# Kernel tuning notes

Hardware: AMD Instinct MI355X
Metric: run time of the kernel (lower is better)

Reference implementation:

```python
import jax, jax.numpy as jnp
import numpy as np
from jax import lax

B, V, C, H, W = 2, 8, 64, 128, 128
A = 256
C3 = 3 * C + 2  # 194 input channels for refine/confidence branches
CO = 3 * C      # 192 output channels of branch_refine
GROUPS = 8      # _group_count(192, 8) == 8
HID = max(4, CO // 4)  # 48 hidden channels in ChannelGate2d


def _conv3(x, w, b):
    y = lax.conv_general_dilated(x, w, (1, 1), 'SAME',
                                 dimension_numbers=('NCHW', 'OIHW', 'NCHW'))
    return y + b[None, :, None, None]


def _group_norm(x, scale, bias, groups, eps=1e-5):
    b, c, h, w = x.shape
    xg = x.reshape(b, groups, c // groups, h, w)
    mu = xg.mean(axis=(2, 3, 4), keepdims=True)
    var = xg.var(axis=(2, 3, 4), keepdims=True)
    xn = ((xg - mu) / jnp.sqrt(var + eps)).reshape(b, c, h, w)
    return xn * scale[None, :, None, None] + bias[None, :, None, None]


def _channel_gate(x, w1, b1, w2, b2):
    pooled = x.mean(axis=(2, 3))                     # [B,C]
    h = jax.nn.silu(pooled @ w1.T + b1)              # [B,HID]
    gate = jax.nn.sigmoid(h @ w2.T + b2)             # [B,C]
    return x * (0.5 + gate)[:, :, None, None]


def _conv_block(x, p):
    h = jax.nn.silu(_group_norm(_conv3(x, p['c1w'], p['c1b']), p['g1s'], p['g1b'], GROUPS))
    h = jax.nn.silu(_group_norm(_conv3(h, p['c2w'], p['c2b']), p['g2s'], p['g2b'], GROUPS))
    h = _channel_gate(h, p['gw1'], p['gb1'], p['gw2'], p['gb2'])
    res = jnp.einsum('bchw,oc->bohw', x, p['rpw']) + p['rpb'][None, :, None, None]
    return h + jnp.tanh(p['rs']) * res


def _fuse(vf, uvs, masks, importance, atlas_size):
    # vf:[B,V,C,H,W] uvs:[B,V,H,W,2] masks:[B,V,1,H,W] importance:[B,V]
    b, v, c, h, w = vf.shape
    P = atlas_size * atlas_size
    weights = jnp.maximum(importance.astype(vf.dtype), 0.0)
    finite = jnp.isfinite(uvs).all(axis=-1)                 # [B,V,H,W]
    valid = (masks[:, :, 0] > 0.5) & finite & (weights[:, :, None, None] > 0.0)
    safe = jnp.where(finite[..., None], uvs, 0.0)
    xi = jnp.round(jnp.clip(safe[..., 0], 0.0, 1.0) * (atlas_size - 1)).astype(jnp.int32)
    yi = jnp.round((1.0 - jnp.clip(safe[..., 1], 0.0, 1.0)) * (atlas_size - 1)).astype(jnp.int32)
    idx = (yi * atlas_size + xi).reshape(b, v * h * w)      # [B,N]
    wvalid = valid.astype(vf.dtype) * weights[:, :, None, None]
    feat = (vf * wvalid[:, :, None]).transpose(0, 2, 1, 3, 4).reshape(b, c, v * h * w)
    cnt = wvalid.reshape(b, v * h * w)

    def per_sample(f, cc, i):
        atlas = jax.ops.segment_sum(f.T, i, num_segments=P).T   # [C,P]
        counts = jax.ops.segment_sum(cc, i, num_segments=P)     # [P]
        return atlas, counts

    atlas, counts = jax.vmap(per_sample)(feat, cnt, idx)
    atlas = atlas.reshape(b, c, atlas_size, atlas_size)
    counts = counts.reshape(b, 1, atlas_size, atlas_size)
    fused = atlas / jnp.maximum(counts, 1.0)
    return fused, (counts > 0).astype(vf.dtype)


def _normalize_per_sample(t, eps=1e-6):
    scale = jnp.maximum(t.reshape(t.shape[0], -1).max(axis=1), eps)
    return jnp.clip(t / scale[:, None, None, None], 0.0, 1.0)


def setup_inputs() -> dict:
    key = jax.random.key(0)
    ks = jax.random.split(key, 20)
    inp = {
        'encoded_views': jax.random.normal(ks[0], (B, V, C, H, W), jnp.float32),
        'view_uvs': jax.random.uniform(ks[1], (B, V, H, W, 2), jnp.float32),
        'view_masks': jax.random.uniform(ks[2], (B, V, 1, H, W), jnp.float32),
        'w_global': jax.random.uniform(ks[3], (B, V), jnp.float32),
        'w_boundary': jax.random.uniform(ks[4], (B, V), jnp.float32),
        'w_highlight': jax.random.uniform(ks[5], (B, V), jnp.float32),
        'atlas_size': A,
        # ConvBlock params (random instead of zero-init so all paths are exercised)
        'c1w': jax.random.normal(ks[6], (CO, C3, 3, 3), jnp.float32) * 0.02,
        'c1b': jnp.zeros((CO,), jnp.float32),
        'g1s': jnp.ones((CO,), jnp.float32),
        'g1b': jnp.zeros((CO,), jnp.float32),
        'c2w': jax.random.normal(ks[7], (CO, CO, 3, 3), jnp.float32) * 0.02,
        'c2b': jnp.zeros((CO,), jnp.float32),
        'g2s': jnp.ones((CO,), jnp.float32),
        'g2b': jnp.zeros((CO,), jnp.float32),
        'gw1': jax.random.normal(ks[8], (HID, CO), jnp.float32) * 0.05,
        'gb1': jnp.zeros((HID,), jnp.float32),
        'gw2': jax.random.normal(ks[9], (CO, HID), jnp.float32) * 0.05,
        'gb2': jnp.zeros((CO,), jnp.float32),
        'rpw': jax.random.normal(ks[10], (CO, C3), jnp.float32) * 0.05,
        'rpb': jnp.zeros((CO,), jnp.float32),
        'rs': jnp.array(0.3, jnp.float32),
        'conf_w': jax.random.normal(ks[11], (3, C3), jnp.float32) * 0.05,
        'conf_b': jnp.zeros((3,), jnp.float32),
        'mix_scale': jnp.array(0.5, jnp.float32),
    }
    return inp


def reference(encoded_views, view_uvs, view_masks, w_global, w_boundary, w_highlight,
              atlas_size, c1w, c1b, g1s, g1b, c2w, c2b, g2s, g2b,
              gw1, gb1, gw2, gb2, rpw, rpb, rs, conf_w, conf_b, mix_scale):
    p = dict(c1w=c1w, c1b=c1b, g1s=g1s, g1b=g1b, c2w=c2w, c2b=c2b, g2s=g2s, g2b=g2b,
             gw1=gw1, gb1=gb1, gw2=gw2, gb2=gb2, rpw=rpw, rpb=rpb, rs=rs)
    g_feat, g_val = _fuse(encoded_views, view_uvs, view_masks, w_global, atlas_size)
    b_feat, b_val = _fuse(encoded_views, view_uvs, view_masks, w_boundary, atlas_size)
    h_feat, h_val = _fuse(encoded_views, view_uvs, view_masks, w_highlight, atlas_size)
    coverage = jnp.clip((g_val + b_val + h_val) / 3.0, 0.0, 1.0)
    stack = jnp.stack([g_feat, b_feat, h_feat], axis=1)     # [B,3,C,A,A]
    uncertainty = jnp.sqrt(stack.var(axis=1).mean(axis=1, keepdims=True))
    uncertainty = _normalize_per_sample(uncertainty) * coverage
    ctx = jnp.concatenate([g_feat, b_feat, h_feat, coverage, uncertainty], axis=1)
    refine = _conv_block(ctx, p)
    rg, rb, rh = jnp.split(refine, 3, axis=1)
    conf = jax.nn.sigmoid(jnp.einsum('bchw,oc->bohw', ctx, conf_w) + conf_b[None, :, None, None])
    ms = jnp.tanh(mix_scale)
    g_out = g_feat + ms * rg * conf[:, 0:1]
    b_out = b_feat + ms * rb * conf[:, 1:2]
    h_out = h_feat + ms * rh * conf[:, 2:3]
    return (g_out, b_out, h_out, coverage, uncertainty, conf)
```

## Files before the change

### kernel.cpp

```cpp
#include <hip/hip_runtime.h>
#include <math.h>

#define B_ 2
#define V_ 8
#define C_ 64
#define HW_ 16384
#define A_ 256
#define P_ 65536
#define CO_ 192
#define CPG_ 24
#define NG_ 8
#define ICP1 224
#define ICP2 192

#define OFF_ACC   0ull
#define SZ_ACC    (2ull*65536*192*4)
#define OFF_CNT   (OFF_ACC + SZ_ACC)
#define SZ_CNT    (2ull*3*65536*4)
#define OFF_CTXB  (OFF_CNT + SZ_CNT)
#define SZ_CTXB   (2ull*65536*224*2)
#define OFF_H1A   (OFF_CTXB + SZ_CTXB)
#define SZ_H1A    (2ull*65536*192*2)
#define OFF_W1    (OFF_H1A + SZ_H1A)
#define SZ_W1     (9ull*192*224*2)
#define OFF_W2    (OFF_W1 + SZ_W1)
#define SZ_W2     (9ull*192*192*2)
#define OFF_SM    (OFF_W2 + SZ_W2 + 256)

#define SM_STATS1 0
#define SM_STATS2 256
#define SM_SCALE  512
#define SM_POOLED 1024
#define SM_GATE   2560
#define SM_RAWU   8192

#define OUT_B    8388608
#define OUT_COV  25165824
#define OUT_UNC  25296896
#define OUT_CONF 25427968

typedef __attribute__((ext_vector_type(4))) float f32x4;
typedef __attribute__((ext_vector_type(8))) short bf16x8;

__device__ __forceinline__ float sigmoidf_(float x){ return 1.f/(1.f+expf(-x)); }
__device__ __forceinline__ float bf2f(unsigned short h){ return __uint_as_float(((unsigned)h)<<16); }
__device__ __forceinline__ unsigned short f2bf(float f){
  unsigned u = __float_as_uint(f);
  return (unsigned short)((u + 0x7fffu + ((u>>16)&1u)) >> 16);
}

__device__ __forceinline__ void gl_lds16(const void* g, void* l){
  __builtin_amdgcn_global_load_lds((const __attribute__((address_space(1))) void*)g,
                                   (__attribute__((address_space(3))) void*)l, 16, 0, 0);
}

__global__ __launch_bounds__(256) void k_prep(const float* __restrict__ c1w,
    const float* __restrict__ c2w, unsigned short* __restrict__ w1p, unsigned short* __restrict__ w2p)
{
  int idx = blockIdx.x*256 + threadIdx.x;
  const int N1 = 9*192*224;
  if (idx < N1){
    int ic = idx % 224; int oc = (idx/224) % 192; int k = idx/(224*192);
    float v = (ic < 194) ? c1w[(size_t)(oc*194+ic)*9 + k] : 0.f;
    w1p[idx] = f2bf(v);
  } else {
    int i2 = idx - N1;
    if (i2 < 9*192*192){
      int ic = i2 % 192; int oc = (i2/192) % 192; int k = i2/(192*192);
      w2p[i2] = f2bf(c2w[(size_t)(oc*192+ic)*9 + k]);
    }
  }
}

__global__ __launch_bounds__(256) void k_fuse(const float* __restrict__ vf,
    const float* __restrict__ uvs, const float* __restrict__ masks,
    const float* __restrict__ wgp, const float* __restrict__ wbp, const float* __restrict__ whp,
    float* __restrict__ acc, float* __restrict__ cnt)
{
  __shared__ __align__(16) float sf[64*65];
  __shared__ int sidx[64];
  __shared__ int svalid[64];
  __shared__ float sw[3];
  int t = threadIdx.x;
  int pix0 = blockIdx.x*64;
  int b   = pix0 / (V_*HW_);
  int rem = pix0 % (V_*HW_);
  int v   = rem / HW_;
  int p2  = rem % HW_;
  size_t vbase = ((size_t)(b*V_+v))*C_*HW_;
  for (int i=0;i<16;i++){
    int f = t + i*256;
    int c = f>>6, px = f&63;
    sf[c*65+px] = vf[vbase + (size_t)c*HW_ + p2 + px];
  }
  if (t<64){
    const float* u2 = uvs + (((size_t)(b*V_+v))*HW_ + p2 + t)*2;
    float ux = u2[0], uy = u2[1];
    int fin = isfinite(ux) && isfinite(uy);
    float su = fin?ux:0.f, svv = fin?uy:0.f;
    float cu = fminf(fmaxf(su,0.f),1.f);
    float cv = fminf(fmaxf(svv,0.f),1.f);
    int xi = (int)rintf(cu*255.f);
    int yi = (int)rintf((1.f-cv)*255.f);
    sidx[t] = yi*256+xi;
    float m = masks[((size_t)(b*V_+v))*HW_ + p2 + t];
    svalid[t] = (m>0.5f) && fin;
  }
  if (t<3){
    const float* wp = (t==0)?wgp:((t==1)?wbp:whp);
    sw[t] = fmaxf(wp[b*V_+v], 0.f);
  }
  __syncthreads();
  int wave = t>>6, lane = t&63;
  float w0 = sw[0], w1 = sw[1], w2 = sw[2];
  for (int i=0;i<16;i++){
    int px = wave*16+i;
    if (!svalid[px]) continue;
    int bin = sidx[px];
    float val = sf[lane*65+px];
    size_t base = ((size_t)b*P_ + bin)*192;
    if (w0>0.f) atomicAdd(&acc[base + lane],        val*w0);
    if (w1>0.f) atomicAdd(&acc[base + 64 + lane],   val*w1);
    if (w2>0.f) atomicAdd(&acc[base + 128 + lane],  val*w2);
    if (lane<3){
      float wv = sw[lane];
      if (wv>0.f) atomicAdd(&cnt[((size_t)(b*3+lane))*P_ + bin], wv);
    }
  }
}

__global__ __launch_bounds__(256) void k_finalize(const float* __restrict__ acc,
      const float* __restrict__ cnt, unsigned short* __restrict__ ctxb,
      float* __restrict__ out_cov, float* __restrict__ raw_unc, int* __restrict__ scale)
{
  __shared__ __align__(16) float sv[64*193];
  __shared__ float sc[3][64];
  __shared__ float up[256];
  __shared__ float s_cov[64];
  __shared__ float s_unc[64];
  int t = threadIdx.x;
  int bin0 = blockIdx.x*64;
  int b = bin0 >> 16;
  int p0 = bin0 & 65535;
  size_t abase = ((size_t)b*P_ + p0)*192;
  for (int i=0;i<48;i++){
    int f = t + i*256;
    int bl = f/192, c = f - bl*192;
    sv[bl*193+c] = acc[abase + f];
  }
  if (t<192){
    int br = t>>6, bl = t&63;
    sc[br][bl] = cnt[((size_t)(b*3+br))*P_ + p0 + bl];
  }
  __syncthreads();
  {
    int bl = t>>2, q = t&3;
    float dg = 1.f/fmaxf(sc[0][bl],1.f);
    float db = 1.f/fmaxf(sc[1][bl],1.f);
    float dh = 1.f/fmaxf(sc[2][bl],1.f);
    float s = 0.f;
    for (int j=0;j<16;j++){
      int c = q*16+j;
      float fg = sv[bl*193+c]*dg;
      float fb = sv[bl*193+64+c]*db;
      float fh = sv[bl*193+128+c]*dh;
      sv[bl*193+c]=fg; sv[bl*193+64+c]=fb; sv[bl*193+128+c]=fh;
      float m = (fg+fb+fh)*(1.f/3.f);
      float d0=fg-m, d1=fb-m, d2=fh-m;
      s += d0*d0+d1*d1+d2*d2;
    }
    up[t] = s;
  }
  __syncthreads();
  if (t<64){
    float tot = up[t*4]+up[t*4+1]+up[t*4+2]+up[t*4+3];
    float u = sqrtf(tot*(1.f/192.f));
    float vg = sc[0][t]>0.f?1.f:0.f;
    float vb = sc[1][t]>0.f?1.f:0.f;
    float vh = sc[2][t]>0.f?1.f:0.f;
    float cov = fminf(fmaxf((vg+vb+vh)*(1.f/3.f),0.f),1.f);
    s_cov[t] = cov; s_unc[t] = u;
    out_cov[(size_t)b*P_ + p0 + t] = cov;
    raw_unc[(size_t)b*P_ + p0 + t] = u;
    atomicMax(&scale[b], __float_as_int(u));
  }
  __syncthreads();
  for (int f=t; f<1792; f+=256){
    int cg = f % 28, bl = f / 28;
    int c0 = cg*8;
    unsigned short h[8];
    #pragma unroll
    for (int j=0;j<8;j++){
      int c = c0+j;
      float vv;
      if (c < 192)      vv = sv[bl*193+c];
      else if (c==192)  vv = s_cov[bl];
      else if (c==193)  vv = s_unc[bl];
      else              vv = 0.f;
      h[j] = f2bf(vv);
    }
    *(uint4*)&ctxb[((size_t)b*P_ + p0 + bl)*ICP1 + c0] = *(uint4*)h;
  }
}

__global__ __launch_bounds__(256) void k_norm_unc(unsigned short* __restrict__ ctxb,
    const int* __restrict__ scale, const float* __restrict__ raw_unc,
    const float* __restrict__ out_cov, float* __restrict__ out_unc)
{
  int tid = blockIdx.x*256 + threadIdx.x;
  int b = tid >> 16;
  float s = fmaxf(__int_as_float(scale[b]), 1e-6f);
  float u = raw_unc[tid];
  float cov = out_cov[tid];
  float un = fminf(fmaxf(u/s,0.f),1.f)*cov;
  out_unc[tid] = un;
  ctxb[(size_t)tid*ICP1 + 193] = f2bf(un);
}

template<int ICP, int CHUNKS>
__global__ __launch_bounds__(256,2) void k_conv3(const unsigned short* __restrict__ X,
    const unsigned short* __restrict__ Wp, const float* __restrict__ bias, float* __restrict__ Y,
    double* __restrict__ stats)
{
  __shared__ short s_in[2][258*32];
  __shared__ short s_w[2][192*32];
  __shared__ float sred[2][64];
  __shared__ float gsm[16];
  int t = threadIdx.x;
  int f_ = blockIdx.x + 256*(blockIdx.y + 3*blockIdx.z);
  int xcd = f_ & 7; int g_ = f_ >> 3;
  int y0  = xcd*32 + (g_ & 31);
  int h_  = g_ >> 5;
  int b   = h_ & 1;
  int oc0 = (h_ >> 1)*64;
  int wv = t>>6, lane = t&63, l15 = lane&15, quad = lane>>4;

  f32x4 acc[4][4];
  #pragma unroll
  for (int mt=0;mt<4;mt++){
    float4 bv = *(const float4*)&bias[oc0 + mt*16 + quad*4];
    f32x4 iv; iv.x=bv.x; iv.y=bv.y; iv.z=bv.z; iv.w=bv.w;
    #pragma unroll
    for (int nt=0;nt<4;nt++) acc[mt][nt]=iv;
  }

  const unsigned short* Xb = X + (size_t)b*P_*ICP;
  int kyLo = (y0==0)?1:0;
  int kyHi = (y0==255)?1:2;
  int nky  = kyHi - kyLo + 1;
  int NP   = CHUNKS*nky;

  if (t < 128){
    int bufi = t>>6, j = t&63;
    int idx = (j<32) ? j : (257*32 + (j-32));
    s_in[bufi][idx] = 0;
  }
  if (t < 128) sred[t>>6][t&63] = 0.f;
  if (t < 16)  gsm[t] = 0.f;

  auto stage = [&](int p, int bufi){
    int ch = p / nky; int ky = kyLo + (p - ch*nky);
    int ic0 = ch*32;
    int gy = y0 + ky - 1;
    const unsigned short* src = Xb + ((size_t)gy*256)*ICP + ic0;
    #pragma unroll
    for (int i=0;i<4;i++){
      int f = t + i*256;
      int xi = 1 + (f>>2), icq = f&3;
      int icg = icq ^ ((xi>>1)&3);
      gl_lds16(src + (size_t)(xi-1)*ICP + icg*8, &s_in[bufi][32 + f*8]);
    }
    const unsigned short* wsrc = Wp + ((size_t)(ky*3)*192 + oc0)*ICP + ic0;
    #pragma unroll
    for (int i=0;i<3;i++){
      int f = t + i*256;
      int kx = f>>8, oc = (f>>2)&63, icq = f&3;
      int r = kx*64 + oc;
      int icg = icq ^ ((r>>1)&3);
      gl_lds16(wsrc + (size_t)(kx*192 + oc)*ICP + icg*8, &s_w[bufi][f*8]);
    }
  };

  stage(0, 0);
  if (NP > 1) stage(1, 1);
  asm volatile("s_waitcnt lgkmcnt(0)" ::: "memory");

  for (int p=0; p<NP; ++p){
    if (p+1 < NP) asm volatile("s_waitcnt vmcnt(7)" ::: "memory");
    else          asm volatile("s_waitcnt vmcnt(0)" ::: "memory");
    __builtin_amdgcn_s_barrier();
    __builtin_amdgcn_sched_barrier(0);
    {
      const short* si = &s_in[p&1][0];
      const short* sw = &s_w[p&1][0];
      #pragma unroll
      for (int kx=0;kx<3;kx++){
        bf16x8 Af[4], Bf[4];
        #pragma unroll
        for (int mt=0;mt<4;mt++){
          int r = kx*64 + mt*16 + l15;
          Af[mt] = *(const bf16x8*)&sw[r*32 + ((quad ^ ((r>>1)&3))&3)*8];
        }
        #pragma unroll
        for (int nt=0;nt<4;nt++){
          int r = wv*64 + nt*16 + l15 + kx;
          Bf[nt] = *(const bf16x8*)&si[r*32 + ((quad ^ ((r>>1)&3))&3)*8];
        }
        #pragma unroll
        for (int mt=0;mt<4;mt++)
          #pragma unroll
          for (int nt=0;nt<4;nt++)
            acc[mt][nt] = __builtin_amdgcn_mfma_f32_16x16x32_bf16(Af[mt], Bf[nt], acc[mt][nt], 0, 0, 0);
      }
    }
    __builtin_amdgcn_s_barrier();
    __builtin_amdgcn_sched_barrier(0);
    if (p+2 < NP) stage(p+2, p&1);
  }

  float* Yb = Y + (size_t)b*P_*192;
  #pragma unroll
  for (int mt=0;mt<4;mt++){
    int oc = oc0 + mt*16 + quad*4;
    #pragma unroll
    for (int nt=0;nt<4;nt++){
      int px = wv*64 + nt*16 + l15;
      *(f32x4*)&Yb[(size_t)(y0*256+px)*192 + oc] = acc[mt][nt];
    }
  }

  #pragma unroll
  for (int mt=0;mt<4;mt++)
    #pragma unroll
    for (int j=0;j<4;j++){
      float v1 = acc[mt][0][j]+acc[mt][1][j]+acc[mt][2][j]+acc[mt][3][j];
      float v2 = acc[mt][0][j]*acc[mt][0][j]+acc[mt][1][j]*acc[mt][1][j]
               + acc[mt][2][j]*acc[mt][2][j]+acc[mt][3][j]*acc[mt][3][j];
      v1 += __shfl_xor(v1,1); v1 += __shfl_xor(v1,2); v1 += __shfl_xor(v1,4); v1 += __shfl_xor(v1,8);
      v2 += __shfl_xor(v2,1); v2 += __shfl_xor(v2,2); v2 += __shfl_xor(v2,4); v2 += __shfl_xor(v2,8);
      if (l15==0){
        int ocl = mt*16 + quad*4 + j;
        atomicAdd(&sred[0][ocl], v1);
        atomicAdd(&sred[1][ocl], v2);
      }
    }
  __syncthreads();
  if (t < 64){
    int g = (oc0 + t)/24;
    atomicAdd(&gsm[g*2],   sred[0][t]);
    atomicAdd(&gsm[g*2+1], sred[1][t]);
  }
  __syncthreads();
  if (t < 8){
    int glo = oc0/24, ghi = (oc0+63)/24;
    if (t >= glo && t <= ghi){
      atomicAdd(&stats[(b*8+t)*2],   (double)gsm[t*2]);
      atomicAdd(&stats[(b*8+t)*2+1], (double)gsm[t*2+1]);
    }
  }
}

__global__ __launch_bounds__(256) void k_gn1_apply(const float* __restrict__ x, const double* __restrict__ stats,
    const float* __restrict__ gs, const float* __restrict__ gb, unsigned short* __restrict__ y)
{
  size_t i8 = ((size_t)blockIdx.x*256 + threadIdx.x)*8;
  int b = (int)(i8 / ((size_t)192*P_));
  int c = (int)(i8 % 192);
  int bg = b*8 + c/24;
  const double N = 24.0*65536.0;
  double mu = stats[bg*2]/N;
  double var = stats[bg*2+1]/N - mu*mu;
  float rstd = 1.0f/sqrtf((float)var + 1e-5f);
  float mean = (float)mu;
  float4 sA = *(const float4*)&gs[c];
  float4 sB = *(const float4*)&gs[c+4];
  float4 bA = *(const float4*)&gb[c];
  float4 bB = *(const float4*)&gb[c+4];
  float4 v0 = *(const float4*)&x[i8];
  float4 v1 = *(const float4*)&x[i8+4];
  float xin[8] = {v0.x,v0.y,v0.z,v0.w,v1.x,v1.y,v1.z,v1.w};
  float scl[8] = {sA.x,sA.y,sA.z,sA.w,sB.x,sB.y,sB.z,sB.w};
  float bia[8] = {bA.x,bA.y,bA.z,bA.w,bB.x,bB.y,bB.z,bB.w};
  unsigned short h[8];
  #pragma unroll
  for (int i=0;i<8;i++){
    float xn = (xin[i]-mean)*rstd*scl[i] + bia[i];
    h[i] = f2bf(xn*sigmoidf_(xn));
  }
  *(uint4*)&y[i8] = *(uint4*)h;
}

__global__ __launch_bounds__(256) void k_gn2_apply(float* __restrict__ x, const double* __restrict__ stats,
    const float* __restrict__ gs, const float* __restrict__ gb, float* __restrict__ pooled)
{
  __shared__ float pl[384];
  int t = threadIdx.x;
  for (int f=t; f<384; f+=256) pl[f]=0.f;
  int tid = blockIdx.x*256 + t;
  int c = (tid*8) % 192;
  float4 sA = *(const float4*)&gs[c];
  float4 sB = *(const float4*)&gs[c+4];
  float4 bA = *(const float4*)&gb[c];
  float4 bB = *(const float4*)&gb[c+4];
  float scl[8] = {sA.x,sA.y,sA.z,sA.w,sB.x,sB.y,sB.z,sB.w};
  float bia[8] = {bA.x,bA.y,bA.z,bA.w,bB.x,bB.y,bB.z,bB.w};
  float mean[2], rstd[2];
  #pragma unroll
  for (int bb=0;bb<2;bb++){
    int bg = bb*8 + c/24;
    const double N = 24.0*65536.0;
    double mu = stats[bg*2]/N;
    double var = stats[bg*2+1]/N - mu*mu;
    rstd[bb] = 1.0f/sqrtf((float)var + 1e-5f);
    mean[bb] = (float)mu;
  }
  float pacc[2][8] = {{0.f}};
  __syncthreads();
  #pragma unroll
  for (int k=0;k<8;k++){
    size_t i8 = ((size_t)tid + (size_t)k*393216)*8;
    int bb = k>>2;
    float4 v0 = *(const float4*)&x[i8];
    float4 v1 = *(const float4*)&x[i8+4];
    float xin[8] = {v0.x,v0.y,v0.z,v0.w,v1.x,v1.y,v1.z,v1.w};
    #pragma unroll
    for (int i=0;i<8;i++){
      float xn = (xin[i]-mean[bb])*rstd[bb]*scl[i] + bia[i];
      xn = xn*sigmoidf_(xn);
      xin[i] = xn;
      pacc[bb][i] += xn;
    }
    *(float4*)&x[i8]   = make_float4(xin[0],xin[1],xin[2],xin[3]);
    *(float4*)&x[i8+4] = make_float4(xin[4],xin[5],xin[6],xin[7]);
  }
  #pragma unroll
  for (int bb=0;bb<2;bb++)
    #pragma unroll
    for (int i=0;i<8;i++) atomicAdd(&pl[bb*192 + c + i], pacc[bb][i]);
  __syncthreads();
  for (int f=t; f<384; f+=256) atomicAdd(&pooled[f], pl[f]*(1.f/65536.f));
}

__global__ void k_gate(const float* __restrict__ pooled, const float* __restrict__ gw1,
    const float* __restrict__ gb1, const float* __restrict__ gw2, const float* __restrict__ gb2,
    float* __restrict__ gatef)
{
  __shared__ float hb[2*48];
  int t = threadIdx.x;
  if (t<96){
    int b=t/48, j=t%48;
    float a = gb1[j];
    for (int c=0;c<192;c++) a = fmaf(pooled[b*192+c], gw1[j*192+c], a);
    hb[t] = a*sigmoidf_(a);
  }
  __syncthreads();
  for (int i=t;i<384;i+=256){
    int b=i/192, c=i%192;
    float a = gb2[c];
    for (int j=0;j<48;j++) a = fmaf(hb[b*48+j], gw2[c*48+j], a);
    gatef[i] = 0.5f + sigmoidf_(a);
  }
}

__global__ __launch_bounds__(256) void k_conf(const unsigned short* __restrict__ ctxb,
    const float* __restrict__ cw, const float* __restrict__ cbias, float* __restrict__ out_conf)
{
  __shared__ float scw[3*224];
  int t = threadIdx.x;
  for (int f=t; f<672; f+=256){
    int c = f % 224, o = f / 224;
    scw[f] = (c<194) ? cw[o*194 + c] : 0.f;
  }
  __syncthreads();
  int tid = blockIdx.x*256 + t;
  int b = tid >> 16, p = tid & 65535;
  const unsigned short* cp = ctxb + ((size_t)b*P_ + p)*ICP1;
  float a0 = cbias[0], a1 = cbias[1], a2 = cbias[2];
  for (int q=0;q<28;q++){
    uint4 v = *(const uint4*)&cp[q*8];
    unsigned wd[4] = {v.x,v.y,v.z,v.w};
    #pragma unroll
    for (int j=0;j<8;j++){
      unsigned bits = wd[j>>1];
      float xf = (j&1) ? __uint_as_float(bits & 0xffff0000u) : __uint_as_float(bits<<16);
      int c = q*8+j;
      a0 = fmaf(xf, scw[c],       a0);
      a1 = fmaf(xf, scw[224+c],   a1);
      a2 = fmaf(xf, scw[448+c],   a2);
    }
  }
  out_conf[((size_t)(b*3+0))*P_ + p] = sigmoidf_(a0);
  out_conf[((size_t)(b*3+1))*P_ + p] = sigmoidf_(a1);
  out_conf[((size_t)(b*3+2))*P_ + p] = sigmoidf_(a2);
}

__global__ __launch_bounds__(256,4) void k_combine(const unsigned short* __restrict__ ctxb,
    const float* __restrict__ h2, const float* __restrict__ rpw, const float* __restrict__ rpb,
    const float* __restrict__ gatef, const float* __restrict__ conf_out,
    const float* __restrict__ rs, const float* __restrict__ mix, float* __restrict__ dout)
{
  __shared__ short s_x[256*32];
  __shared__ short s_w[64*32];
  int t = threadIdx.x;
  size_t p0 = (size_t)blockIdx.x*256;
  int oc0 = blockIdx.y*64, br = blockIdx.y;
  int wv = t>>6, lane = t&63, l15 = lane&15, quad = lane>>4;
  f32x4 acc[4][4];
  #pragma unroll
  for (int mt=0;mt<4;mt++){
    float4 bv = *(const float4*)&rpb[oc0 + mt*16 + quad*4];
    f32x4 iv; iv.x=bv.x; iv.y=bv.y; iv.z=bv.z; iv.w=bv.w;
    #pragma unroll
    for (int nt=0;nt<4;nt++) acc[mt][nt]=iv;
  }
  for (int ch=0; ch<7; ch++){
    int ic0 = ch*32;
    __syncthreads();
    for (int f=t; f<1024; f+=256){
      int icq = f&3, px = f>>2;
      uint4 v = *(const uint4*)&ctxb[(p0+px)*ICP1 + ic0 + icq*8];
      *(uint4*)&s_x[px*32 + ((icq ^ ((px>>1)&3)))*8] = v;
    }
    {
      int oc = t&63, icq = t>>6;
      unsigned short h[8];
      #pragma unroll
      for (int j=0;j<8;j++){
        int ic = ic0 + icq*8 + j;
        h[j] = (ic<194) ? f2bf(rpw[(size_t)(oc0+oc)*194 + ic]) : (unsigned short)0;
      }
      *(uint4*)&s_w[oc*32 + ((icq ^ ((oc>>1)&3)))*8] = *(uint4*)h;
    }
    __syncthreads();
    bf16x8 Af[4], Bf[4];
    #pragma unroll
    for (int mt=0;mt<4;mt++){
      int r = mt*16 + l15;
      Af[mt] = *(const bf16x8*)&s_w[r*32 + (((quad ^ ((r>>1)&3)))&3)*8];
    }
    #pragma unroll
    for (int nt=0;nt<4;nt++){
      int r = wv*64 + nt*16 + l15;
      Bf[nt] = *(const bf16x8*)&s_x[r*32 + (((quad ^ ((r>>1)&3)))&3)*8];
    }
    #pragma unroll
    for (int mt=0;mt<4;mt++)
      #pragma unroll
      for (int nt=0;nt<4;nt++)
        acc[mt][nt] = __builtin_amdgcn_mfma_f32_16x16x32_bf16(Af[mt], Bf[nt], acc[mt][nt], 0, 0, 0);
  }
  float trs = tanhf(rs[0]);
  float ms2 = tanhf(mix[0]);
  int b = (int)(p0 >> 16);
  #pragma unroll
  for (int mt=0;mt<4;mt++){
    int oc = oc0 + mt*16 + quad*4;
    int cc = oc & 63;
    float4 gv = *(const float4*)&gatef[b*192 + oc];
    #pragma unroll
    for (int nt=0;nt<4;nt++){
      size_t pf = p0 + wv*64 + nt*16 + l15;
      int p = (int)(pf & 65535);
      ushort4 fh = *(const ushort4*)&ctxb[pf*ICP1 + oc];
      float4 hv = *(const float4*)&h2[pf*192 + oc];
      float cf = conf_out[((size_t)(b*3+br))*P_ + p];
      size_t dst = (size_t)br*OUT_B + ((size_t)(b*64+cc))*P_ + p;
      dout[dst]            = bf2f(fh.x) + ms2*(hv.x*gv.x + trs*acc[mt][nt].x)*cf;
      dout[dst + P_]       = bf2f(fh.y) + ms2*(hv.y*gv.y + trs*acc[mt][nt].y)*cf;
      dout[dst + 2*P_]     = bf2f(fh.z) + ms2*(hv.z*gv.z + trs*acc[mt][nt].z)*cf;
      dout[dst + 3*P_]     = bf2f(fh.w) + ms2*(hv.w*gv.w + trs*acc[mt][nt].w)*cf;
    }
  }
}

extern "C" void kernel_launch(void* const* d_in, const int* in_sizes, int n_in,
                              void* d_out, int out_size, void* d_ws, size_t ws_size,
                              hipStream_t stream)
{
  const float* vf    = (const float*)d_in[0];
  const float* uvs   = (const float*)d_in[1];
  const float* masks = (const float*)d_in[2];
  const float* wg    = (const float*)d_in[3];
  const float* wb    = (const float*)d_in[4];
  const float* wh    = (const float*)d_in[5];
  const float* c1w = (const float*)d_in[7];
  const float* c1b = (const float*)d_in[8];
  const float* g1s = (const float*)d_in[9];
  const float* g1b = (const float*)d_in[10];
  const float* c2w = (const float*)d_in[11];
  const float* c2b = (const float*)d_in[12];
  const float* g2s = (const float*)d_in[13];
  const float* g2b = (const float*)d_in[14];
  const float* gw1 = (const float*)d_in[15];
  const float* gb1 = (const float*)d_in[16];
  const float* gw2 = (const float*)d_in[17];
  const float* gb2 = (const float*)d_in[18];
  const float* rpw = (const float*)d_in[19];
  const float* rpb = (const float*)d_in[20];
  const float* rs  = (const float*)d_in[21];
  const float* cw  = (const float*)d_in[22];
  const float* cb  = (const float*)d_in[23];
  const float* mix = (const float*)d_in[24];

  char* ws = (char*)d_ws;
  float*          accb  = (float*)(ws + OFF_ACC);
  float*          cntb  = (float*)(ws + OFF_CNT);
  unsigned short* ctxb  = (unsigned short*)(ws + OFF_CTXB);
  unsigned short* h1act = (unsigned short*)(ws + OFF_H1A);
  unsigned short* w1p   = (unsigned short*)(ws + OFF_W1);
  unsigned short* w2p   = (unsigned short*)(ws + OFF_W2);
  float*  h1raw  = (float*)(ws + OFF_ACC);
  float*  h2     = (float*)(ws + OFF_ACC);
  double* stats1 = (double*)(ws + OFF_SM + SM_STATS1);
  double* stats2 = (double*)(ws + OFF_SM + SM_STATS2);
  int*    scale  = (int*)(ws + OFF_SM + SM_SCALE);
  float*  pooled = (float*)(ws + OFF_SM + SM_POOLED);
  float*  gatef  = (float*)(ws + OFF_SM + SM_GATE);
  float*  rawu   = (float*)(ws + OFF_SM + SM_RAWU);

  float* out = (float*)d_out;
  float* out_cov  = out + OUT_COV;
  float* out_unc  = out + OUT_UNC;
  float* out_conf = out + OUT_CONF;

  hipMemsetAsync(ws + OFF_ACC, 0, SZ_ACC + SZ_CNT, stream);
  hipMemsetAsync(ws + OFF_SM, 0, 8192, stream);

  k_prep<<<2808, 256, 0, stream>>>(c1w, c2w, w1p, w2p);
  k_fuse<<<4096, 256, 0, stream>>>(vf, uvs, masks, wg, wb, wh, accb, cntb);
  k_finalize<<<2048, 256, 0, stream>>>(accb, cntb, ctxb, out_cov, rawu, scale);
  k_norm_unc<<<512, 256, 0, stream>>>(ctxb, scale, rawu, out_cov, out_unc);
  k_conv3<ICP1,7><<<dim3(256,3,2), 256, 0, stream>>>(ctxb, w1p, c1b, h1raw, stats1);
  k_gn1_apply<<<12288, 256, 0, stream>>>(h1raw, stats1, g1s, g1b, h1act);
  k_conv3<ICP2,6><<<dim3(256,3,2), 256, 0, stream>>>(h1act, w2p, c2b, h2, stats2);
  k_gn2_apply<<<1536, 256, 0, stream>>>(h2, stats2, g2s, g2b, pooled);
  k_gate<<<1, 256, 0, stream>>>(pooled, gw1, gb1, gw2, gb2, gatef);
  k_conf<<<512, 256, 0, stream>>>(ctxb, cw, cb, out_conf);
  k_combine<<<dim3(512,3), 256, 0, stream>>>(ctxb, h2, rpw, rpb, gatef, out_conf, rs, mix, out);
}
```

Measured before the change: 774.4 us.

## Compute two output rows per conv block to reuse input and weight tiles

```diff
diff --git a/kernel.cpp b/kernel.cpp
--- a/kernel.cpp
+++ b/kernel.cpp
@@ -223,32 +223,29 @@
     double* __restrict__ stats)
 {
   __shared__ short s_in[2][258*32];
-  __shared__ short s_w[2][192*32];
+  __shared__ short s_w[576*32];
   __shared__ float sred[2][64];
   __shared__ float gsm[16];
   int t = threadIdx.x;
-  int f_ = blockIdx.x + 256*(blockIdx.y + 3*blockIdx.z);
+  int f_ = blockIdx.x + 128*(blockIdx.y + 3*blockIdx.z);
   int xcd = f_ & 7; int g_ = f_ >> 3;
-  int y0  = xcd*32 + (g_ & 31);
-  int h_  = g_ >> 5;
+  int ypair = xcd*16 + (g_ & 15);
+  int h_  = g_ >> 4;
   int b   = h_ & 1;
   int oc0 = (h_ >> 1)*64;
+  int y0  = ypair*2;
   int wv = t>>6, lane = t&63, l15 = lane&15, quad = lane>>4;
 
-  f32x4 acc[4][4];
+  f32x4 accA[4][4], accB[4][4];
   #pragma unroll
   for (int mt=0;mt<4;mt++){
     float4 bv = *(const float4*)&bias[oc0 + mt*16 + quad*4];
     f32x4 iv; iv.x=bv.x; iv.y=bv.y; iv.z=bv.z; iv.w=bv.w;
     #pragma unroll
-    for (int nt=0;nt<4;nt++) acc[mt][nt]=iv;
+    for (int nt=0;nt<4;nt++){ accA[mt][nt]=iv; accB[mt][nt]=iv; }
   }
 
   const unsigned short* Xb = X + (size_t)b*P_*ICP;
-  int kyLo = (y0==0)?1:0;
-  int kyHi = (y0==255)?1:2;
-  int nky  = kyHi - kyLo + 1;
-  int NP   = CHUNKS*nky;
 
   if (t < 128){
     int bufi = t>>6, j = t&63;
@@ -258,64 +255,108 @@
   if (t < 128) sred[t>>6][t&63] = 0.f;
   if (t < 16)  gsm[t] = 0.f;
 
-  auto stage = [&](int p, int bufi){
-    int ch = p / nky; int ky = kyLo + (p - ch*nky);
-    int ic0 = ch*32;
-    int gy = y0 + ky - 1;
-    const unsigned short* src = Xb + ((size_t)gy*256)*ICP + ic0;
+  auto issue_input = [&](int c2, int j2){
+    int gy = y0 - 1 + j2;
+    gy = min(max(gy,0),255);
+    const unsigned short* src = Xb + ((size_t)gy*256)*ICP + c2*32;
+    short* dst = &s_in[j2&1][0];
     #pragma unroll
     for (int i=0;i<4;i++){
       int f = t + i*256;
       int xi = 1 + (f>>2), icq = f&3;
       int icg = icq ^ ((xi>>1)&3);
-      gl_lds16(src + (size_t)(xi-1)*ICP + icg*8, &s_in[bufi][32 + f*8]);
-    }
-    const unsigned short* wsrc = Wp + ((size_t)(ky*3)*192 + oc0)*ICP + ic0;
+      gl_lds16(src + (size_t)(xi-1)*ICP + icg*8, dst + 32 + (size_t)f*8);
+    }
+  };
+  auto issue_wa = [&](int c2){
+    int ic0n = c2*32;
+    #pragma unroll
+    for (int i=0;i<6;i++){
+      int f = t + i*256;
+      int oc = (f>>2)&63, icq = f&3;
+      int r = i*64 + oc;
+      int icg = icq ^ ((r>>1)&3);
+      gl_lds16(Wp + ((size_t)(i*192) + oc0 + oc)*ICP + ic0n + icg*8, &s_w[(size_t)f*8]);
+    }
+  };
+  auto issue_wb = [&](int c2){
+    int ic0n = c2*32;
     #pragma unroll
     for (int i=0;i<3;i++){
       int f = t + i*256;
-      int kx = f>>8, oc = (f>>2)&63, icq = f&3;
-      int r = kx*64 + oc;
+      int oc = (f>>2)&63, icq = f&3;
+      int r = (6+i)*64 + oc;
       int icg = icq ^ ((r>>1)&3);
-      gl_lds16(wsrc + (size_t)(kx*192 + oc)*ICP + icg*8, &s_w[bufi][f*8]);
+      gl_lds16(Wp + ((size_t)((6+i)*192) + oc0 + oc)*ICP + ic0n + icg*8, &s_w[(size_t)(1536+f)*8]);
     }
   };
 
-  stage(0, 0);
-  if (NP > 1) stage(1, 1);
+  issue_wa(0);
+  issue_input(0,0);
+  issue_wb(0);
+  issue_input(0,1);
   asm volatile("s_waitcnt lgkmcnt(0)" ::: "memory");
 
-  for (int p=0; p<NP; ++p){
-    if (p+1 < NP) asm volatile("s_waitcnt vmcnt(7)" ::: "memory");
-    else          asm volatile("s_waitcnt vmcnt(0)" ::: "memory");
-    __builtin_amdgcn_s_barrier();
-    __builtin_amdgcn_sched_barrier(0);
-    {
-      const short* si = &s_in[p&1][0];
-      const short* sw = &s_w[p&1][0];
-      #pragma unroll
-      for (int kx=0;kx<3;kx++){
-        bf16x8 Af[4], Bf[4];
+  for (int c=0; c<CHUNKS; ++c){
+    #pragma unroll
+    for (int j=0;j<4;++j){
+      if (j==0)      asm volatile("s_waitcnt vmcnt(7)" ::: "memory");
+      else if (j==1) asm volatile("s_waitcnt vmcnt(4)" ::: "memory");
+      else if (j==2) asm volatile("s_waitcnt vmcnt(4)" ::: "memory");
+      else {
+        if (c==CHUNKS-1) asm volatile("s_waitcnt vmcnt(0)"  ::: "memory");
+        else             asm volatile("s_waitcnt vmcnt(10)" ::: "memory");
+      }
+      __builtin_amdgcn_s_barrier();
+      __builtin_amdgcn_sched_barrier(0);
+
+      bool doA = (j<=2) && (y0 + j >= 1);
+      bool doB = (j>=1) && (y0 - 1 + j <= 255);
+      const short* si = &s_in[j&1][0];
+      if (doA || doB){
         #pragma unroll
-        for (int mt=0;mt<4;mt++){
-          int r = kx*64 + mt*16 + l15;
-          Af[mt] = *(const bf16x8*)&sw[r*32 + ((quad ^ ((r>>1)&3))&3)*8];
+        for (int kx=0;kx<3;kx++){
+          bf16x8 Bf[4];
+          #pragma unroll
+          for (int nt=0;nt<4;nt++){
+            int r = wv*64 + nt*16 + l15 + kx;
+            Bf[nt] = *(const bf16x8*)&si[r*32 + ((quad ^ ((r>>1)&3)))*8];
+          }
+          if (doA){
+            bf16x8 Af[4];
+            #pragma unroll
+            for (int mt=0;mt<4;mt++){
+              int r = j*192 + kx*64 + mt*16 + l15;
+              Af[mt] = *(const bf16x8*)&s_w[r*32 + ((quad ^ ((r>>1)&3)))*8];
+            }
+            #pragma unroll
+            for (int mt=0;mt<4;mt++)
+              #pragma unroll
+              for (int nt=0;nt<4;nt++)
+                accA[mt][nt] = __builtin_amdgcn_mfma_f32_16x16x32_bf16(Af[mt], Bf[nt], accA[mt][nt], 0, 0, 0);
+          }
+          if (doB){
+            bf16x8 Af[4];
+            #pragma unroll
+            for (int mt=0;mt<4;mt++){
+              int r = (j-1)*192 + kx*64 + mt*16 + l15;
+              Af[mt] = *(const bf16x8*)&s_w[r*32 + ((quad ^ ((r>>1)&3)))*8];
+            }
+            #pragma unroll
+            for (int mt=0;mt<4;mt++)
+              #pragma unroll
+              for (int nt=0;nt<4;nt++)
+                accB[mt][nt] = __builtin_amdgcn_mfma_f32_16x16x32_bf16(Af[mt], Bf[nt], accB[mt][nt], 0, 0, 0);
+          }
         }
-        #pragma unroll
-        for (int nt=0;nt<4;nt++){
-          int r = wv*64 + nt*16 + l15 + kx;
-          Bf[nt] = *(const bf16x8*)&si[r*32 + ((quad ^ ((r>>1)&3))&3)*8];
-        }
-        #pragma unroll
-        for (int mt=0;mt<4;mt++)
-          #pragma unroll
-          for (int nt=0;nt<4;nt++)
-            acc[mt][nt] = __builtin_amdgcn_mfma_f32_16x16x32_bf16(Af[mt], Bf[nt], acc[mt][nt], 0, 0, 0);
       }
-    }
-    __builtin_amdgcn_s_barrier();
-    __builtin_amdgcn_sched_barrier(0);
-    if (p+2 < NP) stage(p+2, p&1);
+      __builtin_amdgcn_s_barrier();
+      __builtin_amdgcn_sched_barrier(0);
+      if (j==2 && c+1<CHUNKS) issue_wa(c+1);
+      if (j==3 && c+1<CHUNKS) issue_wb(c+1);
+      if (!(c==CHUNKS-1 && j>=2))
+        issue_input(j>=2 ? c+1 : c, (j+2)&3);
+    }
   }
 
   float* Yb = Y + (size_t)b*P_*192;
@@ -325,21 +366,25 @@
     #pragma unroll
     for (int nt=0;nt<4;nt++){
       int px = wv*64 + nt*16 + l15;
-      *(f32x4*)&Yb[(size_t)(y0*256+px)*192 + oc] = acc[mt][nt];
+      *(f32x4*)&Yb[(size_t)(y0*256+px)*192 + oc]     = accA[mt][nt];
+      *(f32x4*)&Yb[(size_t)((y0+1)*256+px)*192 + oc] = accB[mt][nt];
     }
   }
 
   #pragma unroll
   for (int mt=0;mt<4;mt++)
     #pragma unroll
-    for (int j=0;j<4;j++){
-      float v1 = acc[mt][0][j]+acc[mt][1][j]+acc[mt][2][j]+acc[mt][3][j];
-      float v2 = acc[mt][0][j]*acc[mt][0][j]+acc[mt][1][j]*acc[mt][1][j]
-               + acc[mt][2][j]*acc[mt][2][j]+acc[mt][3][j]*acc[mt][3][j];
+    for (int jj=0;jj<4;jj++){
+      float v1 = accA[mt][0][jj]+accA[mt][1][jj]+accA[mt][2][jj]+accA[mt][3][jj]
+               + accB[mt][0][jj]+accB[mt][1][jj]+accB[mt][2][jj]+accB[mt][3][jj];
+      float v2 = accA[mt][0][jj]*accA[mt][0][jj]+accA[mt][1][jj]*accA[mt][1][jj]
+               + accA[mt][2][jj]*accA[mt][2][jj]+accA[mt][3][jj]*accA[mt][3][jj]
+               + accB[mt][0][jj]*accB[mt][0][jj]+accB[mt][1][jj]*accB[mt][1][jj]
+               + accB[mt][2][jj]*accB[mt][2][jj]+accB[mt][3][jj]*accB[mt][3][jj];
       v1 += __shfl_xor(v1,1); v1 += __shfl_xor(v1,2); v1 += __shfl_xor(v1,4); v1 += __shfl_xor(v1,8);
       v2 += __shfl_xor(v2,1); v2 += __shfl_xor(v2,2); v2 += __shfl_xor(v2,4); v2 += __shfl_xor(v2,8);
       if (l15==0){
-        int ocl = mt*16 + quad*4 + j;
+        int ocl = mt*16 + quad*4 + jj;
         atomicAdd(&sred[0][ocl], v1);
         atomicAdd(&sred[1][ocl], v2);
       }
@@ -630,9 +675,9 @@
   k_fuse<<<4096, 256, 0, stream>>>(vf, uvs, masks, wg, wb, wh, accb, cntb);
   k_finalize<<<2048, 256, 0, stream>>>(accb, cntb, ctxb, out_cov, rawu, scale);
   k_norm_unc<<<512, 256, 0, stream>>>(ctxb, scale, rawu, out_cov, out_unc);
-  k_conv3<ICP1,7><<<dim3(256,3,2), 256, 0, stream>>>(ctxb, w1p, c1b, h1raw, stats1);
+  k_conv3<ICP1,7><<<dim3(128,3,2), 256, 0, stream>>>(ctxb, w1p, c1b, h1raw, stats1);
   k_gn1_apply<<<12288, 256, 0, stream>>>(h1raw, stats1, g1s, g1b, h1act);
-  k_conv3<ICP2,6><<<dim3(256,3,2), 256, 0, stream>>>(h1act, w2p, c2b, h2, stats2);
+  k_conv3<ICP2,6><<<dim3(128,3,2), 256, 0, stream>>>(h1act, w2p, c2b, h2, stats2);
   k_gn2_apply<<<1536, 256, 0, stream>>>(h2, stats2, g2s, g2b, pooled);
   k_gate<<<1, 256, 0, stream>>>(pooled, gw1, gb1, gw2, gb2, gatef);
   k_conf<<<512, 256, 0, stream>>>(ctxb, cw, cb, out_conf);
```

After: 758.4 us. -2.1%, faster.
